# Optimization experiments

Hardware: AMD Instinct MI355X
Metric: run time of the kernel (lower is better)

## Reference

```python
import jax, jax.numpy as jnp
import numpy as np

N_NODES = 100000
N_EDGES = 1600000
D_IN = 128
D_HID = 128
D_EMB = 128
D_OUT = 16


def _glorot(key, shape):
    fan_in, fan_out = shape
    lim = (6.0 / (fan_in + fan_out)) ** 0.5
    return jax.random.uniform(key, shape, jnp.float32, -lim, lim)


def setup_inputs() -> dict:
    key = jax.random.key(0)
    ks = jax.random.split(key, 12)
    x = jax.random.normal(ks[0], (N_NODES, D_IN), jnp.float32)
    edge_index = jax.random.randint(ks[1], (2, N_EDGES), 0, N_NODES, jnp.int32)
    return {
        "x": x,
        "edge_index": edge_index,
        # SAGEConv layer 0: neighbor weight, self(root) weight, bias
        "Wn0": _glorot(ks[2], (D_IN, D_HID)),
        "Ws0": _glorot(ks[3], (D_IN, D_HID)),
        "b0": jnp.zeros((D_HID,), jnp.float32),
        # SAGEConv layer 1
        "Wn1": _glorot(ks[4], (D_HID, D_HID)),
        "Ws1": _glorot(ks[5], (D_HID, D_HID)),
        "b1": jnp.zeros((D_HID,), jnp.float32),
        # SAGEConv layer 2 (to embedding dim)
        "Wn2": _glorot(ks[6], (D_HID, D_EMB)),
        "Ws2": _glorot(ks[7], (D_HID, D_EMB)),
        "b2": jnp.zeros((D_EMB,), jnp.float32),
        # final fc
        "Wfc": _glorot(ks[8], (D_EMB, D_OUT)),
        "bfc": jnp.zeros((D_OUT,), jnp.float32),
    }


def _sage_conv(x, src, dst, deg_inv, Wn, Ws, b):
    # mean-aggregate source features at destination nodes, then transform.
    agg = jax.ops.segment_sum(x[src], dst, num_segments=N_NODES)  # [N, d]
    mean = agg * deg_inv[:, None]
    return mean @ Wn + x @ Ws + b


def reference(x, edge_index, Wn0, Ws0, b0, Wn1, Ws1, b1, Wn2, Ws2, b2, Wfc, bfc):
    src, dst = edge_index[0], edge_index[1]
    deg = jax.ops.segment_sum(jnp.ones((src.shape[0],), x.dtype), dst,
                              num_segments=N_NODES)
    deg_inv = 1.0 / jnp.maximum(deg, 1.0)

    h = _sage_conv(x, src, dst, deg_inv, Wn0, Ws0, b0)
    h = jax.nn.relu(h)  # dropout omitted (eval mode / deterministic reference)
    h = _sage_conv(h, src, dst, deg_inv, Wn1, Ws1, b1)
    h = jax.nn.relu(h)
    emb = _sage_conv(h, src, dst, deg_inv, Wn2, Ws2, b2)
    y = emb @ Wfc + bfc
    return emb, jax.nn.log_softmax(y, axis=1)
```

## Files before the change

### kernel.cpp

```cpp
#include <hip/hip_runtime.h>
#include <hip/hip_fp16.h>

#define NN 100000
#define NE 1600000
#define DD 128
#define CAP 64
#define FRAG_ELEMS 16384

typedef __attribute__((ext_vector_type(8))) _Float16 half8;
typedef __attribute__((ext_vector_type(4))) float f32x4;

__global__ void k_xcast(const float* __restrict__ x, _Float16* __restrict__ xh) {
    int t = blockIdx.x * 256 + threadIdx.x;
    const float* p = x + (size_t)t * 8;
    float4 v0 = *(const float4*)p;
    float4 v1 = *(const float4*)(p + 4);
    half8 o = { (_Float16)v0.x, (_Float16)v0.y, (_Float16)v0.z, (_Float16)v0.w,
                (_Float16)v1.x, (_Float16)v1.y, (_Float16)v1.z, (_Float16)v1.w };
    *(half8*)(xh + (size_t)t * 8) = o;
}

__global__ void k_fill(const int* __restrict__ src, const int* __restrict__ dst,
                       int* __restrict__ cnt, int* __restrict__ bkt) {
    int e = blockIdx.x * 256 + threadIdx.x;
    if (e < NE) {
        int d = dst[e];
        int p = atomicAdd(&cnt[d], 1);
        if (p < CAP) bkt[(size_t)d * CAP + p] = src[e];
    }
}

__global__ __launch_bounds__(256) void k_wprep(const float* __restrict__ W0,
                                               const float* __restrict__ W1,
                                               const float* __restrict__ W2,
                                               const float* __restrict__ W3,
                                               const float* __restrict__ W4,
                                               const float* __restrict__ W5,
                                               _Float16* __restrict__ out) {
    int mat = blockIdx.x >> 6;
    int e = (blockIdx.x & 63) * 256 + threadIdx.x;
    const float* W = (mat == 0) ? W0 : (mat == 1) ? W1 : (mat == 2) ? W2
                   : (mat == 3) ? W3 : (mat == 4) ? W4 : W5;
    int j = e & 7;
    int lane = (e >> 3) & 63;
    int ct = (e >> 9) & 7;
    int kt = e >> 12;
    int k = kt * 32 + (lane >> 4) * 8 + j;
    int n = ct * 16 + (lane & 15);
    float v = W[k * 128 + n];
    _Float16 hi = (_Float16)v;
    _Float16 lo = (_Float16)(v - (float)hi);
    _Float16* mb = out + (size_t)mat * 2 * FRAG_ELEMS;
    mb[e] = hi;
    mb[FRAG_ELEMS + e] = lo;
}

__global__ __launch_bounds__(256) void k_agg(const _Float16* __restrict__ h,
                                             const int* __restrict__ cnt,
                                             const int* __restrict__ bkt,
                                             _Float16* __restrict__ mean) {
    int node = blockIdx.x * 4 + (threadIdx.x >> 6);
    if (node >= NN) return;
    int lane = threadIdx.x & 63;
    int q = lane >> 4;
    int col = (lane & 15) * 8;
    int deg = cnt[node];
    int n = deg > CAP ? CAP : deg;
    const int* b = bkt + (size_t)node * CAP;
    float a[8] = {};
    int i = 0;
    for (; i + 8 <= n; i += 8) {
        int s0 = b[i + q];
        int s1 = b[i + 4 + q];
        half8 v0 = *(const half8*)(h + (size_t)s0 * DD + col);
        half8 v1 = *(const half8*)(h + (size_t)s1 * DD + col);
#pragma unroll
        for (int j = 0; j < 8; ++j) a[j] += (float)v0[j] + (float)v1[j];
    }
    if (i + 4 <= n) {
        int s0 = b[i + q];
        half8 v0 = *(const half8*)(h + (size_t)s0 * DD + col);
#pragma unroll
        for (int j = 0; j < 8; ++j) a[j] += (float)v0[j];
        i += 4;
    }
    if (i + q < n) {
        int s = b[i + q];
        half8 v = *(const half8*)(h + (size_t)s * DD + col);
#pragma unroll
        for (int j = 0; j < 8; ++j) a[j] += (float)v[j];
    }
#pragma unroll
    for (int j = 0; j < 8; ++j) {
        a[j] += __shfl_xor(a[j], 16);
        a[j] += __shfl_xor(a[j], 32);
    }
    if (q == 0) {
        float di = 1.0f / (float)(deg > 1 ? deg : 1);
        half8 o;
#pragma unroll
        for (int j = 0; j < 8; ++j) o[j] = (_Float16)(a[j] * di);
        *(half8*)(mean + (size_t)node * DD + col) = o;
    }
}

__global__ __launch_bounds__(256) void k_gemm(
    const _Float16* __restrict__ meanp, const _Float16* __restrict__ hin,
    const _Float16* __restrict__ wf,
    const float* __restrict__ bias,
    _Float16* __restrict__ outh, float* __restrict__ outf) {

    int t = threadIdx.x;
    int wave = t >> 6;
    int lane = t & 63;
    int m16 = lane & 15;
    int kg = lane >> 4;
    int rowA = blockIdx.x * 64 + wave * 16 + m16;
    if (rowA >= NN) rowA = NN - 1;

    f32x4 acc[8] = {};

#pragma unroll
    for (int s = 0; s < 2; ++s) {
        const _Float16* Whi = wf + s * 2 * FRAG_ELEMS;
        const _Float16* Wlo = Whi + FRAG_ELEMS;
        const _Float16* Ap = (s ? hin : meanp) + (size_t)rowA * DD;
#pragma unroll
        for (int kt = 0; kt < 4; ++kt) {
            half8 a = *(const half8*)(Ap + kt * 32 + kg * 8);
#pragma unroll
            for (int ct = 0; ct < 8; ++ct) {
                int off = ((kt * 8 + ct) * 64 + lane) * 8;
                half8 bh = *(const half8*)(Whi + off);
                half8 bl = *(const half8*)(Wlo + off);
                acc[ct] = __builtin_amdgcn_mfma_f32_16x16x32_f16(a, bh, acc[ct], 0, 0, 0);
                acc[ct] = __builtin_amdgcn_mfma_f32_16x16x32_f16(a, bl, acc[ct], 0, 0, 0);
            }
        }
    }

    int rbase = blockIdx.x * 64 + wave * 16 + kg * 4;
    if (outh) {
#pragma unroll
        for (int ct = 0; ct < 8; ++ct) {
            int col = ct * 16 + m16;
            float bv = bias[col];
#pragma unroll
            for (int i = 0; i < 4; ++i) {
                int r = rbase + i;
                if (r < NN)
                    outh[(size_t)r * DD + col] = (_Float16)fmaxf(acc[ct][i] + bv, 0.0f);
            }
        }
    } else {
#pragma unroll
        for (int ct = 0; ct < 8; ++ct) {
            int col = ct * 16 + m16;
            float bv = bias[col];
#pragma unroll
            for (int i = 0; i < 4; ++i) {
                int r = rbase + i;
                if (r < NN)
                    outf[(size_t)r * DD + col] = acc[ct][i] + bv;
            }
        }
    }
}

__global__ __launch_bounds__(256) void k_fc(const float* __restrict__ emb,
                                            const float* __restrict__ Wfc,
                                            const float* __restrict__ bfc,
                                            float* __restrict__ out) {
    __shared__ float se[16 * 128];
    __shared__ float swt[128 * 16];
    int t = threadIdx.x;
    int nb = blockIdx.x * 16;
    int idx = t * 8;
    *(float4*)(se + idx)      = *(const float4*)(emb + (size_t)nb * 128 + idx);
    *(float4*)(se + idx + 4)  = *(const float4*)(emb + (size_t)nb * 128 + idx + 4);
    *(float4*)(swt + idx)     = *(const float4*)(Wfc + idx);
    *(float4*)(swt + idx + 4) = *(const float4*)(Wfc + idx + 4);
    __syncthreads();

    int nl = t >> 4;
    int o = t & 15;
    float acc = bfc[o];
    const float* er = se + nl * 128;
#pragma unroll 8
    for (int k = 0; k < 128; ++k)
        acc += er[k] * swt[k * 16 + o];

    float m = acc;
#pragma unroll
    for (int d = 1; d < 16; d <<= 1) m = fmaxf(m, __shfl_xor(m, d, 16));
    float e = expf(acc - m);
    float ssum = e;
#pragma unroll
    for (int d = 1; d < 16; d <<= 1) ssum += __shfl_xor(ssum, d, 16);
    out[(size_t)(nb + nl) * 16 + o] = (acc - m) - logf(ssum);
}

extern "C" void kernel_launch(void* const* d_in, const int* in_sizes, int n_in,
                              void* d_out, int out_size, void* d_ws, size_t ws_size,
                              hipStream_t stream) {
    const float* x   = (const float*)d_in[0];
    const int*   ei  = (const int*)d_in[1];
    const float* Wn0 = (const float*)d_in[2];
    const float* Ws0 = (const float*)d_in[3];
    const float* b0  = (const float*)d_in[4];
    const float* Wn1 = (const float*)d_in[5];
    const float* Ws1 = (const float*)d_in[6];
    const float* b1  = (const float*)d_in[7];
    const float* Wn2 = (const float*)d_in[8];
    const float* Ws2 = (const float*)d_in[9];
    const float* b2  = (const float*)d_in[10];
    const float* Wfc = (const float*)d_in[11];
    const float* bfc = (const float*)d_in[12];

    const int* src = ei;
    const int* dst = ei + NE;

    float* emb_out = (float*)d_out;
    float* lsm_out = emb_out + (size_t)NN * 128;

    char* ws = (char*)d_ws;
    _Float16* xh    = (_Float16*)(ws);
    _Float16* hA    = (_Float16*)(ws + 25600000);
    _Float16* hB    = (_Float16*)(ws + 51200000);
    _Float16* mean  = (_Float16*)(ws + 76800000);
    int*      cnt   = (int*)     (ws + 102400000);
    int*      bkt   = (int*)     (ws + 102800000);
    _Float16* wfrag = (_Float16*)(ws + 128400000);

    hipMemsetAsync(cnt, 0, NN * sizeof(int), stream);
    k_xcast<<<(NN * DD / 8) / 256, 256, 0, stream>>>(x, xh);
    k_wprep<<<384, 256, 0, stream>>>(Wn0, Ws0, Wn1, Ws1, Wn2, Ws2, wfrag);
    k_fill<<<(NE + 255) / 256, 256, 0, stream>>>(src, dst, cnt, bkt);

    const int agg_blocks  = (NN + 3) / 4;
    const int gemm_blocks = (NN + 63) / 64;
    _Float16* wf0 = wfrag;
    _Float16* wf1 = wfrag + 4 * FRAG_ELEMS;
    _Float16* wf2 = wfrag + 8 * FRAG_ELEMS;

    k_agg<<<agg_blocks, 256, 0, stream>>>(xh, cnt, bkt, mean);
    k_gemm<<<gemm_blocks, 256, 0, stream>>>(mean, xh, wf0, b0, hA, nullptr);

    k_agg<<<agg_blocks, 256, 0, stream>>>(hA, cnt, bkt, mean);
    k_gemm<<<gemm_blocks, 256, 0, stream>>>(mean, hA, wf1, b1, hB, nullptr);

    k_agg<<<agg_blocks, 256, 0, stream>>>(hB, cnt, bkt, mean);
    k_gemm<<<gemm_blocks, 256, 0, stream>>>(mean, hB, wf2, b2, nullptr, emb_out);

    k_fc<<<NN / 16, 256, 0, stream>>>(emb_out, Wfc, bfc, lsm_out);
}
```

Measured before the change: 581.5 us.

## Build compact CSR via two-pass binning instead of fixed-capacity buckets

Replaces the per-node atomic fill into 64-slot buckets with a two-pass build. The first pass bins edges into coarse destination bins, each split into eight sub-segments to spread atomic contention. The second pass, one block per bin, computes a prefix sum and scatters the packed sources into a contiguous CSR array through shared memory. The aggregation kernels then read compact, sequential neighbour lists instead of sparse 64-wide rows, which cuts memory footprint and scattered atomics. The cost is an extra kernel and fixed segment and stage capacities (SEGCAP, STAGE_CAP) that can silently drop edges if a bin overflows.

```diff
diff --git a/kernel.cpp b/kernel.cpp
--- a/kernel.cpp
+++ b/kernel.cpp
@@ -4,7 +4,12 @@
 #define NN 100000
 #define NE 1600000
 #define DD 128
-#define CAP 64
+#define NB 500
+#define NPB 200
+#define RSEG 8
+#define SEGCAP 640
+#define SEGTOT (NB*RSEG)
+#define STAGE_CAP 4096
 #define FRAG_ELEMS 16384
 
 typedef __attribute__((ext_vector_type(8))) _Float16 half8;
@@ -20,14 +25,89 @@
     *(half8*)(xh + (size_t)t * 8) = o;
 }
 
-__global__ void k_fill(const int* __restrict__ src, const int* __restrict__ dst,
-                       int* __restrict__ cnt, int* __restrict__ bkt) {
+__global__ void k_binA(const int* __restrict__ src, const int* __restrict__ dst,
+                       int* __restrict__ segcnt, unsigned int* __restrict__ binbuf) {
     int e = blockIdx.x * 256 + threadIdx.x;
-    if (e < NE) {
-        int d = dst[e];
-        int p = atomicAdd(&cnt[d], 1);
-        if (p < CAP) bkt[(size_t)d * CAP + p] = src[e];
-    }
+    if (e >= NE) return;
+    int s = src[e];
+    int d = dst[e];
+    int bin = d / NPB;
+    int local = d - bin * NPB;
+    int seg = bin * RSEG + (e & (RSEG - 1));
+    int p = atomicAdd(&segcnt[seg], 1);
+    if (p < SEGCAP) binbuf[(size_t)seg * SEGCAP + p] = (unsigned)s | ((unsigned)local << 17);
+}
+
+__global__ __launch_bounds__(256) void k_binB(const int* __restrict__ segcnt,
+                                              const unsigned int* __restrict__ binbuf,
+                                              int* __restrict__ offs, int* __restrict__ csr) {
+    __shared__ int red[256];
+    __shared__ int lcnt[NPB], lofs[NPB], lcur[NPB];
+    __shared__ unsigned int stage[STAGE_CAP];
+    int bin = blockIdx.x;
+    int t = threadIdx.x;
+    int lim = bin * RSEG;
+
+    int part = 0;
+    for (int i = t; i < lim; i += 256) {
+        int c = segcnt[i];
+        part += (c > SEGCAP ? SEGCAP : c);
+    }
+    red[t] = part;
+    if (t < NPB) lcnt[t] = 0;
+    __syncthreads();
+    for (int d = 128; d; d >>= 1) {
+        if (t < d) red[t] += red[t + d];
+        __syncthreads();
+    }
+    int base = red[0];
+    __syncthreads();
+
+    int m[RSEG];
+#pragma unroll
+    for (int k = 0; k < RSEG; ++k) {
+        int c = segcnt[lim + k];
+        m[k] = c > SEGCAP ? SEGCAP : c;
+    }
+
+#pragma unroll
+    for (int k = 0; k < RSEG; ++k) {
+        const unsigned int* sb = binbuf + (size_t)(lim + k) * SEGCAP;
+        for (int i = t; i < m[k]; i += 256) atomicAdd(&lcnt[sb[i] >> 17], 1);
+    }
+    __syncthreads();
+
+    int v = (t < NPB) ? lcnt[t] : 0;
+    red[t] = v;
+    __syncthreads();
+    for (int d = 1; d < 256; d <<= 1) {
+        int u = (t >= d) ? red[t - d] : 0;
+        __syncthreads();
+        red[t] += u;
+        __syncthreads();
+    }
+    if (t < NPB) { lofs[t] = red[t] - v; lcur[t] = 0; }
+    int mtot = red[255];
+    __syncthreads();
+
+    if (t < NPB) offs[bin * NPB + t] = base + lofs[t];
+    if (bin == NB - 1 && t == 0) offs[NN] = base + mtot;
+
+#pragma unroll
+    for (int k = 0; k < RSEG; ++k) {
+        const unsigned int* sb = binbuf + (size_t)(lim + k) * SEGCAP;
+        for (int i = t; i < m[k]; i += 256) {
+            unsigned int p = sb[i];
+            int local = p >> 17;
+            int q = atomicAdd(&lcur[local], 1);
+            int pos = lofs[local] + q;
+            if (pos < STAGE_CAP) stage[pos] = p & 0x1FFFFu;
+        }
+    }
+    __syncthreads();
+
+    int lim2 = mtot > STAGE_CAP ? STAGE_CAP : mtot;
+    for (int i = t; i < lim2; i += 256) csr[base + i] = (int)stage[i];
 }
 
 __global__ __launch_bounds__(256) void k_wprep(const float* __restrict__ W0,
@@ -56,17 +136,18 @@
 }
 
 __global__ __launch_bounds__(256) void k_agg(const _Float16* __restrict__ h,
-                                             const int* __restrict__ cnt,
-                                             const int* __restrict__ bkt,
+                                             const int* __restrict__ offs,
+                                             const int* __restrict__ csr,
                                              _Float16* __restrict__ mean) {
     int node = blockIdx.x * 4 + (threadIdx.x >> 6);
     if (node >= NN) return;
     int lane = threadIdx.x & 63;
     int q = lane >> 4;
     int col = (lane & 15) * 8;
-    int deg = cnt[node];
-    int n = deg > CAP ? CAP : deg;
-    const int* b = bkt + (size_t)node * CAP;
+    int beg = offs[node];
+    int end = offs[node + 1];
+    int n = end - beg;
+    const int* b = csr + beg;
     float a[8] = {};
     int i = 0;
     for (; i + 8 <= n; i += 8) {
@@ -96,7 +177,7 @@
         a[j] += __shfl_xor(a[j], 32);
     }
     if (q == 0) {
-        float di = 1.0f / (float)(deg > 1 ? deg : 1);
+        float di = 1.0f / (float)(n > 1 ? n : 1);
         half8 o;
 #pragma unroll
         for (int j = 0; j < 8; ++j) o[j] = (_Float16)(a[j] * di);
@@ -224,18 +305,21 @@
     float* lsm_out = emb_out + (size_t)NN * 128;
 
     char* ws = (char*)d_ws;
-    _Float16* xh    = (_Float16*)(ws);
-    _Float16* hA    = (_Float16*)(ws + 25600000);
-    _Float16* hB    = (_Float16*)(ws + 51200000);
-    _Float16* mean  = (_Float16*)(ws + 76800000);
-    int*      cnt   = (int*)     (ws + 102400000);
-    int*      bkt   = (int*)     (ws + 102800000);
-    _Float16* wfrag = (_Float16*)(ws + 128400000);
-
-    hipMemsetAsync(cnt, 0, NN * sizeof(int), stream);
+    _Float16*     xh     = (_Float16*)(ws);
+    _Float16*     hA     = (_Float16*)(ws + 25600000);
+    _Float16*     hB     = (_Float16*)(ws + 51200000);
+    _Float16*     mean   = (_Float16*)(ws + 76800000);
+    int*          segcnt = (int*)     (ws + 102400000);
+    int*          offs   = (int*)     (ws + 102416000);
+    unsigned int* binbuf = (unsigned int*)(ws + 102816064);
+    int*          csr    = (int*)     (ws + 113056064);
+    _Float16*     wfrag  = (_Float16*)(ws + 119456064);
+
+    hipMemsetAsync(segcnt, 0, SEGTOT * sizeof(int), stream);
+    k_binA<<<(NE + 255) / 256, 256, 0, stream>>>(src, dst, segcnt, binbuf);
     k_xcast<<<(NN * DD / 8) / 256, 256, 0, stream>>>(x, xh);
     k_wprep<<<384, 256, 0, stream>>>(Wn0, Ws0, Wn1, Ws1, Wn2, Ws2, wfrag);
-    k_fill<<<(NE + 255) / 256, 256, 0, stream>>>(src, dst, cnt, bkt);
+    k_binB<<<NB, 256, 0, stream>>>(segcnt, binbuf, offs, csr);
 
     const int agg_blocks  = (NN + 3) / 4;
     const int gemm_blocks = (NN + 63) / 64;
@@ -243,13 +327,13 @@
     _Float16* wf1 = wfrag + 4 * FRAG_ELEMS;
     _Float16* wf2 = wfrag + 8 * FRAG_ELEMS;
 
-    k_agg<<<agg_blocks, 256, 0, stream>>>(xh, cnt, bkt, mean);
+    k_agg<<<agg_blocks, 256, 0, stream>>>(xh, offs, csr, mean);
     k_gemm<<<gemm_blocks, 256, 0, stream>>>(mean, xh, wf0, b0, hA, nullptr);
 
-    k_agg<<<agg_blocks, 256, 0, stream>>>(hA, cnt, bkt, mean);
+    k_agg<<<agg_blocks, 256, 0, stream>>>(hA, offs, csr, mean);
     k_gemm<<<gemm_blocks, 256, 0, stream>>>(mean, hA, wf1, b1, hB, nullptr);
 
-    k_agg<<<agg_blocks, 256, 0, stream>>>(hB, cnt, bkt, mean);
+    k_agg<<<agg_blocks, 256, 0, stream>>>(hB, offs, csr, mean);
     k_gemm<<<gemm_blocks, 256, 0, stream>>>(mean, hB, wf2, b2, nullptr, emb_out);
 
     k_fc<<<NN / 16, 256, 0, stream>>>(emb_out, Wfc, bfc, lsm_out);
```

New measurement: 598.5 us. +2.9%, slower.
